# Kernel optimization log

Hardware: AMD Instinct MI355X
Metric: run time of the kernel (lower is better)

## Reference

```python
import jax, jax.numpy as jnp
import numpy as np

B, N, D = 2, 2048, 768
H = 12
HD = D // H
HID = 4 * D
SCALE = HD ** -0.5
EPS = 1e-5


def layer_norm(x, g, b):
    mu = jnp.mean(x, axis=-1, keepdims=True)
    var = jnp.var(x, axis=-1, keepdims=True)
    return (x - mu) * jax.lax.rsqrt(var + EPS) * g + b


def setup_inputs() -> dict:
    key = jax.random.key(0)
    ks = jax.random.split(key, 12)
    s = 0.02
    return {
        "x": jax.random.normal(ks[0], (B, N, D), jnp.float32),
        "att_mask": jax.random.randint(ks[1], (B, N), 0, 2, jnp.int32),
        "ln1_g": jnp.ones((D,), jnp.float32),
        "ln1_b": jnp.zeros((D,), jnp.float32),
        "qkv_w": jax.random.normal(ks[2], (3 * D, D), jnp.float32) * s,
        "q_bias": jnp.zeros((D,), jnp.float32),
        "v_bias": jnp.zeros((D,), jnp.float32),
        "proj_w": jax.random.normal(ks[3], (D, D), jnp.float32) * s,
        "proj_b": jnp.zeros((D,), jnp.float32),
        "ln2_g": jnp.ones((D,), jnp.float32),
        "ln2_b": jnp.zeros((D,), jnp.float32),
        "fc1_w": jax.random.normal(ks[4], (HID, D), jnp.float32) * s,
        "fc1_b": jnp.zeros((HID,), jnp.float32),
        "fc2_w": jax.random.normal(ks[5], (D, HID), jnp.float32) * s,
        "fc2_b": jnp.zeros((D,), jnp.float32),
        "gamma_1": 0.1 * jnp.ones((D,), jnp.float32),
        "gamma_2": 0.1 * jnp.ones((D,), jnp.float32),
    }


def reference(x, att_mask, ln1_g, ln1_b, qkv_w, q_bias, v_bias, proj_w, proj_b,
              ln2_g, ln2_b, fc1_w, fc1_b, fc2_w, fc2_b, gamma_1, gamma_2):
    # --- attention branch ---
    h = layer_norm(x, ln1_g, ln1_b)
    qkv_bias = jnp.concatenate([q_bias, jnp.zeros_like(v_bias), v_bias])
    qkv = h @ qkv_w.T + qkv_bias                      # [B,N,3D]
    qkv = qkv.reshape(B, N, 3, H, HD).transpose(2, 0, 3, 1, 4)
    q, k, v = qkv[0], qkv[1], qkv[2]                  # [B,H,N,HD]
    logit = jnp.einsum('bhqd,bhkd->bhqk', q * SCALE, k)
    mask = att_mask[:, None, None, :]                 # key mask [B,1,1,N]
    logit = jnp.where(mask == 0, -jnp.inf, logit)
    attn = jax.nn.softmax(logit, axis=-1)
    o = jnp.einsum('bhqk,bhkd->bhqd', attn, v)
    o = o.transpose(0, 2, 1, 3).reshape(B, N, D)
    o = o @ proj_w.T + proj_b
    x = x + gamma_1 * o
    # --- mlp branch ---
    h2 = layer_norm(x, ln2_g, ln2_b)
    h2 = jax.nn.gelu(h2 @ fc1_w.T + fc1_b, approximate=False)
    h2 = h2 @ fc2_w.T + fc2_b
    return x + gamma_2 * h2
```

## Files before the change

kernel.cpp:

```cpp
#include <hip/hip_runtime.h>
#include <hip/hip_bf16.h>
#include <stdint.h>

typedef __bf16 bf16x8 __attribute__((ext_vector_type(8)));
typedef __bf16 bf16x2 __attribute__((ext_vector_type(2)));
typedef unsigned short u16x8 __attribute__((ext_vector_type(8)));
typedef float f32x4 __attribute__((ext_vector_type(4)));
typedef float f32x16 __attribute__((ext_vector_type(16)));
typedef uint32_t u32x4 __attribute__((ext_vector_type(4)));

#define DMODEL 768
#define NSEQ   2048
#define BATCH  2
#define NHEAD  12
#define HDIM   64
#define HIDDEN 3072
#define PROWS  (BATCH * NHEAD * NSEQ)
#define NZ     4
#define QSCALE 0.18033688011112042f
#define MCONST 16.0f
#define PMASKED 1.52587890625e-05f

__device__ __forceinline__ uint16_t f2bf(float f) {
  __bf16 h = (__bf16)f;
  return __builtin_bit_cast(uint16_t, h);
}
__device__ __forceinline__ float bf2f(uint16_t u) {
  uint32_t x = (uint32_t)u << 16;
  return __builtin_bit_cast(float, x);
}
__device__ __forceinline__ bf16x8 ldb8(const uint16_t* p) {
  return __builtin_bit_cast(bf16x8, *reinterpret_cast<const u16x8*>(p));
}
__device__ __forceinline__ float gelu_f(float x) {
  float u = x * (1.0f + 0.044715f * x * x);
  float e = fminf(u * 2.302208545f, 80.0f);
  float t = exp2f(e);
  return x * t / (t + 1.0f);
}
__device__ __forceinline__ void xcd_swz(int& bx, int& by) {
  const int gx = gridDim.x;
  const int nwg = gx * gridDim.y;
  const int orig = blockIdx.y * gx + blockIdx.x;
  const int wg = (orig & 7) * (nwg >> 3) + (orig >> 3);
  bx = wg % gx;
  by = wg / gx;
}

using as1_void = __attribute__((address_space(1))) const void;
using as3_void = __attribute__((address_space(3))) void;
__device__ __forceinline__ void gload16(const uint16_t* src, uint16_t* lds) {
  __builtin_amdgcn_global_load_lds((as1_void*)src, (as3_void*)lds, 16, 0, 0);
}
#define MEMFENCE asm volatile("" ::: "memory")

#define N_QKVW  (3 * DMODEL * DMODEL)
#define N_PROJW (DMODEL * DMODEL)
#define N_FC1W  (HIDDEN * DMODEL)
#define N_FC2W  (DMODEL * HIDDEN)
__global__ __launch_bounds__(256) void cvt4_kernel(const float* __restrict__ s0,
                                                   const float* __restrict__ s1,
                                                   const float* __restrict__ s2,
                                                   const float* __restrict__ s3,
                                                   uint16_t* __restrict__ d0,
                                                   uint16_t* __restrict__ d1,
                                                   uint16_t* __restrict__ d2,
                                                   uint16_t* __restrict__ d3) {
  int i4 = (blockIdx.x * 256 + threadIdx.x) * 4;
  const float* s;
  uint16_t* d;
  if (i4 < N_QKVW) { s = s0 + i4; d = d0 + i4; }
  else if (i4 < N_QKVW + N_PROJW) { int j = i4 - N_QKVW; s = s1 + j; d = d1 + j; }
  else if (i4 < N_QKVW + N_PROJW + N_FC1W) { int j = i4 - N_QKVW - N_PROJW; s = s2 + j; d = d2 + j; }
  else { int j = i4 - N_QKVW - N_PROJW - N_FC1W; s = s3 + j; d = d3 + j; }
  float4 v = *reinterpret_cast<const float4*>(s);
  ushort4 o;
  o.x = f2bf(v.x); o.y = f2bf(v.y); o.z = f2bf(v.z); o.w = f2bf(v.w);
  *reinterpret_cast<ushort4*>(d) = o;
}

__global__ __launch_bounds__(256) void bias_kernel(const float* __restrict__ qb,
                                                   const float* __restrict__ vb,
                                                   float* __restrict__ out) {
  int j = blockIdx.x * 256 + threadIdx.x;
  if (j < 3 * DMODEL) {
    float v = 0.f;
    if (j < DMODEL) v = qb[j];
    else if (j >= 2 * DMODEL) v = vb[j - 2 * DMODEL];
    out[j] = v;
  }
}

__global__ __launch_bounds__(256) void ln_kernel(const float* __restrict__ x,
                                                 const float* __restrict__ g,
                                                 const float* __restrict__ bt,
                                                 uint16_t* __restrict__ out) {
  const int row = blockIdx.x;
  const int t = threadIdx.x;
  const float* xr = x + (size_t)row * DMODEL;
  float v0 = xr[t], v1 = xr[t + 256], v2 = xr[t + 512];
  float s = v0 + v1 + v2;
  float q = v0 * v0 + v1 * v1 + v2 * v2;
  for (int off = 32; off >= 1; off >>= 1) {
    s += __shfl_xor(s, off);
    q += __shfl_xor(q, off);
  }
  __shared__ float ss[4], sq[4];
  int w = t >> 6;
  if ((t & 63) == 0) { ss[w] = s; sq[w] = q; }
  __syncthreads();
  s = ss[0] + ss[1] + ss[2] + ss[3];
  q = sq[0] + sq[1] + sq[2] + sq[3];
  const float mean = s * (1.0f / DMODEL);
  const float var = q * (1.0f / DMODEL) - mean * mean;
  const float rstd = rsqrtf(var + 1e-5f);
  uint16_t* orow = out + (size_t)row * DMODEL;
  orow[t]       = f2bf((v0 - mean) * rstd * g[t]       + bt[t]);
  orow[t + 256] = f2bf((v1 - mean) * rstd * g[t + 256] + bt[t + 256]);
  orow[t + 512] = f2bf((v2 - mean) * rstd * g[t + 512] + bt[t + 512]);
}

template <int MODE>
__global__ __launch_bounds__(256, 3) void gemm128(const uint16_t* __restrict__ A,
                                                  const uint16_t* __restrict__ W,
                                                  const float* __restrict__ bias,
                                                  void* __restrict__ outp,
                                                  uint16_t* __restrict__ km,
                                                  uint16_t* __restrict__ vt,
                                                  const int* __restrict__ amask,
                                                  int M, int N, int K) {
  __shared__ uint16_t As[2][128 * 32];
  __shared__ uint16_t Bs[2][128 * 32];
  const int tid = threadIdx.x;
  const int lane = tid & 63;
  const int w = tid >> 6;
  const int wr = w >> 1, wc = w & 1;
  int bx, by;
  xcd_swz(bx, by);
  const int row0 = by * 128;
  const int col0 = bx * 128;
  const int lr = lane & 15;
  const int g = lane >> 4;

  const int o0 = w * 1024 + lane * 16;
  const int o1 = o0 + 4096;
  const int r0s = o0 >> 6, c0s = (o0 & 63) >> 1;
  const int r1s = o1 >> 6, c1s = (o1 & 63) >> 1;
  const int l0 = (w * 1024) >> 1;
  const int l1 = l0 + 2048;
  const uint16_t* Abase = A + (size_t)row0 * K;
  const uint16_t* Wbase = W + (size_t)col0 * K;

  auto stage = [&](int kt) {
    uint16_t* Ad = &As[kt & 1][0];
    uint16_t* Bd = &Bs[kt & 1][0];
    const int kk = kt * 32;
    gload16(Abase + (size_t)r0s * K + kk + c0s, Ad + l0);
    gload16(Abase + (size_t)r1s * K + kk + c1s, Ad + l1);
    gload16(Wbase + (size_t)r0s * K + kk + c0s, Bd + l0);
    gload16(Wbase + (size_t)r1s * K + kk + c1s, Bd + l1);
  };

  f32x4 acc[4][4] = {};
  const int nt = K >> 5;
  stage(0);
  for (int kt = 0; kt < nt; ++kt) {
    if (kt + 1 < nt) {
      stage(kt + 1);
      asm volatile("s_waitcnt vmcnt(4)" ::: "memory");
    } else {
      asm volatile("s_waitcnt vmcnt(0)" ::: "memory");
    }
    __builtin_amdgcn_s_barrier();
    MEMFENCE;
    const uint16_t* Ab = &As[kt & 1][0];
    const uint16_t* Bb = &Bs[kt & 1][0];
    bf16x8 a[4], b[4];
#pragma unroll
    for (int m = 0; m < 4; ++m) a[m] = ldb8(Ab + (wr * 64 + m * 16 + lr) * 32 + g * 8);
#pragma unroll
    for (int n = 0; n < 4; ++n) b[n] = ldb8(Bb + (wc * 64 + n * 16 + lr) * 32 + g * 8);
#pragma unroll
    for (int m = 0; m < 4; ++m)
#pragma unroll
      for (int n = 0; n < 4; ++n)
        acc[m][n] = __builtin_amdgcn_mfma_f32_16x16x32_bf16(a[m], b[n], acc[m][n], 0, 0, 0);
    MEMFENCE;
    __builtin_amdgcn_s_barrier();
  }

  if constexpr (MODE == 0) {
    const int sect = col0 / DMODEL;
    const int bb = row0 >> 11;
    const int* mrow = amask + bb * NSEQ;
#pragma unroll
    for (int m = 0; m < 4; ++m) {
      int row = row0 + wr * 64 + m * 16 + g * 4;
      int nn = row & 2047;
      int mk[4];
#pragma unroll
      for (int ri = 0; ri < 4; ++ri) mk[ri] = mrow[nn + ri];
#pragma unroll
      for (int n = 0; n < 4; ++n) {
        int col = col0 + wc * 64 + n * 16 + lr;
        float bv = bias[col];
        if (sect == 0) {
#pragma unroll
          for (int ri = 0; ri < 4; ++ri)
            ((uint16_t*)outp)[(size_t)(row + ri) * DMODEL + col] =
                f2bf((acc[m][n][ri] + bv) * QSCALE);
        } else if (sect == 1) {
          int kc = col - DMODEL;
#pragma unroll
          for (int ri = 0; ri < 4; ++ri)
            km[(size_t)(row + ri) * DMODEL + kc] =
                mk[ri] ? f2bf(acc[m][n][ri] + bv) : (uint16_t)0;
        } else {
          int vc = col - 2 * DMODEL;
          int hh2 = vc >> 6, dd = vc & 63;
          ushort4 sv;
          sv.x = mk[0] ? f2bf(acc[m][n][0] + bv) : (uint16_t)0;
          sv.y = mk[1] ? f2bf(acc[m][n][1] + bv) : (uint16_t)0;
          sv.z = mk[2] ? f2bf(acc[m][n][2] + bv) : (uint16_t)0;
          sv.w = mk[3] ? f2bf(acc[m][n][3] + bv) : (uint16_t)0;
          *reinterpret_cast<ushort4*>(
              vt + ((size_t)((bb * NHEAD + hh2) * 64 + dd)) * NSEQ + nn) = sv;
        }
      }
    }
  } else {
#pragma unroll
    for (int m = 0; m < 4; ++m) {
      int row = row0 + wr * 64 + m * 16 + g * 4;
#pragma unroll
      for (int n = 0; n < 4; ++n) {
        int col = col0 + wc * 64 + n * 16 + lr;
        float bv = bias[col];
#pragma unroll
        for (int ri = 0; ri < 4; ++ri) {
          float val = acc[m][n][ri] + bv;
          ((uint16_t*)outp)[(size_t)(row + ri) * N + col] = f2bf(gelu_f(val));
        }
      }
    }
  }
}

__global__ __launch_bounds__(256, 3) void gemm64(const uint16_t* __restrict__ A,
                                                 const uint16_t* __restrict__ W,
                                                 const float* __restrict__ bias,
                                                 float* __restrict__ outp,
                                                 const float* __restrict__ resid,
                                                 const float* __restrict__ gamma,
                                                 int M, int N, int K) {
  __shared__ uint16_t As[2][64 * 64];
  __shared__ uint16_t Bs[2][64 * 64];
  const int tid = threadIdx.x;
  const int lane = tid & 63;
  const int w = tid >> 6;
  const int wr = w >> 1, wc = w & 1;
  int bx, by;
  xcd_swz(bx, by);
  const int row0 = by * 64;
  const int col0 = bx * 64;
  const int lr = lane & 15;
  const int g = lane >> 4;

  const int srow = tid >> 3;
  const int schunk = tid & 7;
  const uint16_t* Abase = A + (size_t)row0 * K;
  const uint16_t* Wbase = W + (size_t)col0 * K;

  auto stage = [&](int kt) {
    uint16_t* Ad = &As[kt & 1][0];
    uint16_t* Bd = &Bs[kt & 1][0];
    const int kk = kt * 64;
#pragma unroll
    for (int i = 0; i < 2; ++i) {
      const int row = i * 32 + srow;
      const int sc = (schunk ^ (row & 7)) * 8;
      gload16(Abase + (size_t)row * K + kk + sc, Ad + i * 2048 + w * 512);
      gload16(Wbase + (size_t)row * K + kk + sc, Bd + i * 2048 + w * 512);
    }
  };

  f32x4 acc[2][2] = {};
  const int nt = K >> 6;
  stage(0);
  for (int kt = 0; kt < nt; ++kt) {
    if (kt + 1 < nt) {
      stage(kt + 1);
      asm volatile("s_waitcnt vmcnt(4)" ::: "memory");
    } else {
      asm volatile("s_waitcnt vmcnt(0)" ::: "memory");
    }
    __builtin_amdgcn_s_barrier();
    MEMFENCE;
    const uint16_t* Ab = &As[kt & 1][0];
    const uint16_t* Bb = &Bs[kt & 1][0];
#pragma unroll
    for (int kk = 0; kk < 2; ++kk) {
      bf16x8 a[2], bf[2];
#pragma unroll
      for (int m = 0; m < 2; ++m) {
        const int row = wr * 32 + m * 16 + lr;
        a[m] = ldb8(Ab + row * 64 + (((kk * 4 + g) ^ (row & 7)) * 8));
      }
#pragma unroll
      for (int n = 0; n < 2; ++n) {
        const int row = wc * 32 + n * 16 + lr;
        bf[n] = ldb8(Bb + row * 64 + (((kk * 4 + g) ^ (row & 7)) * 8));
      }
#pragma unroll
      for (int m = 0; m < 2; ++m)
#pragma unroll
        for (int n = 0; n < 2; ++n)
          acc[m][n] = __builtin_amdgcn_mfma_f32_16x16x32_bf16(a[m], bf[n], acc[m][n], 0, 0, 0);
    }
    MEMFENCE;
    __builtin_amdgcn_s_barrier();
  }

#pragma unroll
  for (int m = 0; m < 2; ++m) {
    int row = row0 + wr * 32 + m * 16 + g * 4;
#pragma unroll
    for (int n = 0; n < 2; ++n) {
      int col = col0 + wc * 32 + n * 16 + lr;
      float bv = bias[col];
      float gv = gamma[col];
#pragma unroll
      for (int ri = 0; ri < 4; ++ri) {
        float val = acc[m][n][ri] + bv;
        size_t idx = (size_t)(row + ri) * N + col;
        outp[idx] = resid[idx] + gv * val;
      }
    }
  }
}

__global__ __launch_bounds__(512, 4) void attn_kernel(const uint16_t* __restrict__ qb_,
                                                      const uint16_t* __restrict__ km,
                                                      const uint16_t* __restrict__ vt,
                                                      const int* __restrict__ mask,
                                                      uint16_t* __restrict__ po,
                                                      float* __restrict__ pml) {
  __shared__ uint16_t Kb[4][64 * 64];
  __shared__ uint16_t Vb[4][64 * 64];
  __shared__ unsigned long long mbits[8];
  const int tid = threadIdx.x;
  const int lane = tid & 63;
  const int w = tid >> 6;
  const int bh = blockIdx.x;
  const int b = bh / NHEAD, hd = bh % NHEAD;
  const int z = blockIdx.z;
  const int kbase = z * 512;
  const int q0 = blockIdx.y * 256 + w * 32;
  const int l31 = lane & 31;
  const int hh = lane >> 5;

  const int* mb = mask + b * NSEQ;
  {
    unsigned long long bm = __ballot(mb[kbase + w * 64 + lane] != 0);
    if (lane == 0) mbits[w] = bm;
  }

  bf16x8 qa[4];
  const uint16_t* qptr = qb_ + (size_t)(b * NSEQ + q0 + l31) * DMODEL + hd * HDIM + hh * 8;
#pragma unroll
  for (int dblk = 0; dblk < 4; ++dblk) qa[dblk] = ldb8(qptr + dblk * 16);

  const uint16_t* kmb = km + (size_t)b * NSEQ * DMODEL + hd * HDIM;
  const uint16_t* vtb = vt + (size_t)bh * HDIM * NSEQ;

  __syncthreads();

  const int srow = tid >> 3;
  const int sxor = ((tid & 7) ^ (srow & 7)) * 8;
  auto stage = [&](int t) {
    const int pb = t & 3;
    const int k0 = kbase + t * 64;
    gload16(kmb + (size_t)(k0 + srow) * DMODEL + sxor, &Kb[pb][w * 512]);
    gload16(vtb + (size_t)srow * NSEQ + k0 + sxor, &Vb[pb][w * 512]);
  };

  u16x8 ones_u;
#pragma unroll
  for (int e = 0; e < 8; ++e) ones_u[e] = 0x3F80;
  const bf16x8 ones = __builtin_bit_cast(bf16x8, ones_u);

  f32x16 oacc[2] = {};
  f32x16 lacc = {};

  stage(0);
  stage(1);
  stage(2);
#pragma unroll
  for (int t = 0; t < 8; ++t) {
    if (t < 6) {
      asm volatile("s_waitcnt vmcnt(4)" ::: "memory");
    } else if (t == 6) {
      asm volatile("s_waitcnt vmcnt(2)" ::: "memory");
    } else {
      asm volatile("s_waitcnt vmcnt(0)" ::: "memory");
    }
    __builtin_amdgcn_s_barrier();
    MEMFENCE;
    if (t + 3 < 8) stage(t + 3);
    const uint16_t* Kbp = &Kb[t & 3][0];
    const uint16_t* Vbp = &Vb[t & 3][0];

    f32x16 st[2];
    __builtin_amdgcn_s_setprio(1);
#pragma unroll
    for (int kblk = 0; kblk < 2; ++kblk) {
      f32x16 acc = {};
      const uint16_t* kr = Kbp + (kblk * 32 + l31) * 64;
#pragma unroll
      for (int dblk = 0; dblk < 4; ++dblk) {
        bf16x8 kf = ldb8(kr + ((dblk * 2 + hh) ^ (l31 & 7)) * 8);
        acc = __builtin_amdgcn_mfma_f32_32x32x16_bf16(kf, qa[dblk], acc, 0, 0, 0);
      }
      st[kblk] = acc;
    }
    __builtin_amdgcn_s_setprio(0);

    uint32_t pk[2][8];
#pragma unroll
    for (int kblk = 0; kblk < 2; ++kblk)
#pragma unroll
      for (int wn = 0; wn < 8; ++wn) {
        float e0 = exp2f(st[kblk][2 * wn] - MCONST);
        float e1 = exp2f(st[kblk][2 * wn + 1] - MCONST);
        bf16x2 pr = {(__bf16)e0, (__bf16)e1};
        pk[kblk][wn] = __builtin_bit_cast(uint32_t, pr);
      }

    bf16x8 af[4];
#pragma unroll
    for (int kb16 = 0; kb16 < 4; ++kb16) {
      const int kblk = kb16 >> 1;
      const int a4 = (kb16 & 1) * 4;
      uint32_t ow0 = hh ? pk[kblk][a4 + 2] : pk[kblk][a4 + 0];
      uint32_t ow1 = hh ? pk[kblk][a4 + 3] : pk[kblk][a4 + 1];
      uint32_t gv0 = hh ? pk[kblk][a4 + 0] : pk[kblk][a4 + 2];
      uint32_t gv1 = hh ? pk[kblk][a4 + 1] : pk[kblk][a4 + 3];
      uint32_t sw0 = (uint32_t)__shfl_xor((int)gv0, 32);
      uint32_t sw1 = (uint32_t)__shfl_xor((int)gv1, 32);
      u32x4 afu;
      afu[0] = hh ? sw0 : ow0;
      afu[1] = hh ? sw1 : ow1;
      afu[2] = hh ? ow0 : sw0;
      afu[3] = hh ? ow1 : sw1;
      af[kb16] = __builtin_bit_cast(bf16x8, afu);
    }

    __builtin_amdgcn_s_setprio(1);
#pragma unroll
    for (int dblk = 0; dblk < 2; ++dblk) {
      const uint16_t* vr = Vbp + (dblk * 32 + l31) * 64;
#pragma unroll
      for (int kb16 = 0; kb16 < 4; ++kb16) {
        bf16x8 vf = ldb8(vr + ((kb16 * 2 + hh) ^ (l31 & 7)) * 8);
        oacc[dblk] = __builtin_amdgcn_mfma_f32_32x32x16_bf16(af[kb16], vf, oacc[dblk], 0, 0, 0);
      }
    }
#pragma unroll
    for (int kb16 = 0; kb16 < 4; ++kb16)
      lacc = __builtin_amdgcn_mfma_f32_32x32x16_bf16(af[kb16], ones, lacc, 0, 0, 0);
    __builtin_amdgcn_s_setprio(0);
    MEMFENCE;
  }

  int cnt = 0;
#pragma unroll
  for (int it = 0; it < 8; ++it) cnt += 64 - __popcll(mbits[it]);
  const float cntf = (float)cnt * PMASKED;

  uint16_t* ob = po + ((size_t)z * PROWS + (size_t)bh * NSEQ + q0) * 64;
#pragma unroll
  for (int r = 0; r < 16; ++r) {
    const int qrow = (r & 3) + 8 * (r >> 2) + 4 * hh;
#pragma unroll
    for (int dblk = 0; dblk < 2; ++dblk)
      ob[(size_t)qrow * 64 + dblk * 32 + l31] = f2bf(oacc[dblk][r]);
  }
  if (l31 == 0) {
#pragma unroll
    for (int r = 0; r < 16; ++r) {
      const int qrow = (r & 3) + 8 * (r >> 2) + 4 * hh;
      pml[(size_t)z * PROWS + (size_t)bh * NSEQ + q0 + qrow] = lacc[r] - cntf;
    }
  }
}

__global__ __launch_bounds__(256) void merge_kernel(const uint16_t* __restrict__ po,
                                                    const float* __restrict__ pml,
                                                    uint16_t* __restrict__ o) {
  int gid = blockIdx.x * 256 + threadIdx.x;
  int row = gid >> 3;
  int c0 = (gid & 7) * 8;
  float L = 0.f;
#pragma unroll
  for (int zz = 0; zz < NZ; ++zz) L += pml[(size_t)zz * PROWS + row];
  float inv = L > 0.f ? 1.f / L : 0.f;
  float sum[8] = {};
#pragma unroll
  for (int zz = 0; zz < NZ; ++zz) {
    u16x8 a = *reinterpret_cast<const u16x8*>(po + ((size_t)zz * PROWS + row) * 64 + c0);
#pragma unroll
    for (int e = 0; e < 8; ++e) sum[e] += bf2f(a[e]);
  }
  int bh = row >> 11, q = row & 2047;
  int bb = bh / NHEAD, hh = bh % NHEAD;
  uint16_t* op = o + ((size_t)(bb * NSEQ + q) * DMODEL + hh * HDIM + c0);
  u16x8 outv;
#pragma unroll
  for (int e = 0; e < 8; ++e) outv[e] = f2bf(sum[e] * inv);
  *reinterpret_cast<u16x8*>(op) = outv;
}

extern "C" void kernel_launch(void* const* d_in, const int* in_sizes, int n_in,
                              void* d_out, int out_size, void* d_ws, size_t ws_size,
                              hipStream_t stream) {
  const float* x      = (const float*)d_in[0];
  const int*   amask  = (const int*)d_in[1];
  const float* ln1_g  = (const float*)d_in[2];
  const float* ln1_b  = (const float*)d_in[3];
  const float* qkv_w  = (const float*)d_in[4];
  const float* q_bias = (const float*)d_in[5];
  const float* v_bias = (const float*)d_in[6];
  const float* proj_w = (const float*)d_in[7];
  const float* proj_b = (const float*)d_in[8];
  const float* ln2_g  = (const float*)d_in[9];
  const float* ln2_b  = (const float*)d_in[10];
  const float* fc1_w  = (const float*)d_in[11];
  const float* fc1_b  = (const float*)d_in[12];
  const float* fc2_w  = (const float*)d_in[13];
  const float* fc2_b  = (const float*)d_in[14];
  const float* g1     = (const float*)d_in[15];
  const float* g2     = (const float*)d_in[16];

  char* ws = (char*)d_ws;
  uint16_t* qkvw_bf  = (uint16_t*)(ws + 0);
  uint16_t* projw_bf = (uint16_t*)(ws + 3538944);
  uint16_t* fc1w_bf  = (uint16_t*)(ws + 4718592);
  uint16_t* fc2w_bf  = (uint16_t*)(ws + 9437184);
  float*    qkvbias  = (float*)(ws + 14155776);
  uint16_t* h_bf     = (uint16_t*)(ws + 14164992);
  uint16_t* q_bf     = (uint16_t*)(ws + 20456448);
  uint16_t* km       = (uint16_t*)(ws + 26747904);
  uint16_t* vt_bf    = (uint16_t*)(ws + 33039360);
  uint16_t* po       = (uint16_t*)(ws + 39330816);
  float*    pml      = (float*)(ws + 64496640);
  uint16_t* o_bf     = q_bf;
  float*    x1_f     = (float*)(ws + 26747904);
  uint16_t* fc1_bf   = (uint16_t*)(ws + 39330816);
  uint16_t* h2_bf    = h_bf;

  const int M = BATCH * NSEQ;

  cvt4_kernel<<<(N_QKVW + N_PROJW + N_FC1W + N_FC2W) / 1024, 256, 0, stream>>>(
      qkv_w, proj_w, fc1_w, fc2_w, qkvw_bf, projw_bf, fc1w_bf, fc2w_bf);
  bias_kernel<<<(3 * DMODEL + 255) / 256, 256, 0, stream>>>(q_bias, v_bias, qkvbias);

  ln_kernel<<<M, 256, 0, stream>>>(x, ln1_g, ln1_b, h_bf);
  gemm128<0><<<dim3((3 * DMODEL) / 128, M / 128), 256, 0, stream>>>(
      h_bf, qkvw_bf, qkvbias, q_bf, km, vt_bf, amask, M, 3 * DMODEL, DMODEL);
  attn_kernel<<<dim3(BATCH * NHEAD, NSEQ / 256, NZ), 512, 0, stream>>>(
      q_bf, km, vt_bf, amask, po, pml);
  merge_kernel<<<(PROWS * 8) / 256, 256, 0, stream>>>(po, pml, o_bf);
  gemm64<<<dim3(DMODEL / 64, M / 64), 256, 0, stream>>>(
      o_bf, projw_bf, proj_b, x1_f, x, g1, M, DMODEL, DMODEL);
  ln_kernel<<<M, 256, 0, stream>>>(x1_f, ln2_g, ln2_b, h2_bf);
  gemm128<2><<<dim3(HIDDEN / 128, M / 128), 256, 0, stream>>>(
      h2_bf, fc1w_bf, fc1_b, fc1_bf, nullptr, nullptr, nullptr, M, HIDDEN, DMODEL);
  gemm64<<<dim3(DMODEL / 64, M / 64), 256, 0, stream>>>(
      fc1_bf, fc2w_bf, fc2_b, (float*)d_out, x1_f, g2, M, DMODEL, HIDDEN);
}
```

Baseline: 180.6 us.

## Compact unmasked keys so attention only iterates over valid key tiles

A new scan kernel computes prefix positions of unmasked keys per batch. The QKV GEMM epilogue scatters K and V rows into compacted positions, and the K/V buffers are zeroed beforehand. Attention then splits only the valid key tiles across its NZ partitions and corrects for padding in the denominator. With a random mask about half the keys are masked, so this is meant to roughly halve attention work, at the cost of extra memsets, a scan launch, and scattered scalar stores in the GEMM epilogue.

```diff
diff --git a/kernel.cpp b/kernel.cpp
--- a/kernel.cpp
+++ b/kernel.cpp
@@ -91,6 +91,31 @@
   }
 }
 
+__global__ __launch_bounds__(256) void scan_kernel(const int* __restrict__ mask,
+                                                   int* __restrict__ pos,
+                                                   int* __restrict__ nk) {
+  const int b = blockIdx.x;
+  const int tid = threadIdx.x;
+  const int lane = tid & 63, w = tid >> 6;
+  __shared__ int wsum[4];
+  int base = 0;
+  for (int c = 0; c < NSEQ; c += 256) {
+    int m = (mask[b * NSEQ + c + tid] != 0);
+    unsigned long long bits = __ballot(m);
+    int lanepre = __popcll(bits & ((1ull << lane) - 1ull));
+    if (lane == 0) wsum[w] = __popcll(bits);
+    __syncthreads();
+    int wpre = 0;
+#pragma unroll
+    for (int i = 0; i < 4; ++i) wpre += (i < w) ? wsum[i] : 0;
+    pos[b * NSEQ + c + tid] = base + wpre + lanepre;
+    int total = wsum[0] + wsum[1] + wsum[2] + wsum[3];
+    __syncthreads();
+    base += total;
+  }
+  if (tid == 0) nk[b] = base;
+}
+
 __global__ __launch_bounds__(256) void ln_kernel(const float* __restrict__ x,
                                                  const float* __restrict__ g,
                                                  const float* __restrict__ bt,
@@ -128,6 +153,7 @@
                                                   uint16_t* __restrict__ km,
                                                   uint16_t* __restrict__ vt,
                                                   const int* __restrict__ amask,
+                                                  const int* __restrict__ pos,
                                                   int M, int N, int K) {
   __shared__ uint16_t As[2][128 * 32];
   __shared__ uint16_t Bs[2][128 * 32];
@@ -193,13 +219,14 @@
     const int sect = col0 / DMODEL;
     const int bb = row0 >> 11;
     const int* mrow = amask + bb * NSEQ;
+    const int* prow = pos + bb * NSEQ;
 #pragma unroll
     for (int m = 0; m < 4; ++m) {
       int row = row0 + wr * 64 + m * 16 + g * 4;
       int nn = row & 2047;
-      int mk[4];
-#pragma unroll
-      for (int ri = 0; ri < 4; ++ri) mk[ri] = mrow[nn + ri];
+      int mk[4], ps[4];
+#pragma unroll
+      for (int ri = 0; ri < 4; ++ri) { mk[ri] = mrow[nn + ri]; ps[ri] = prow[nn + ri]; }
 #pragma unroll
       for (int n = 0; n < 4; ++n) {
         int col = col0 + wc * 64 + n * 16 + lr;
@@ -213,18 +240,15 @@
           int kc = col - DMODEL;
 #pragma unroll
           for (int ri = 0; ri < 4; ++ri)
-            km[(size_t)(row + ri) * DMODEL + kc] =
-                mk[ri] ? f2bf(acc[m][n][ri] + bv) : (uint16_t)0;
+            if (mk[ri])
+              km[(size_t)(bb * NSEQ + ps[ri]) * DMODEL + kc] = f2bf(acc[m][n][ri] + bv);
         } else {
           int vc = col - 2 * DMODEL;
           int hh2 = vc >> 6, dd = vc & 63;
-          ushort4 sv;
-          sv.x = mk[0] ? f2bf(acc[m][n][0] + bv) : (uint16_t)0;
-          sv.y = mk[1] ? f2bf(acc[m][n][1] + bv) : (uint16_t)0;
-          sv.z = mk[2] ? f2bf(acc[m][n][2] + bv) : (uint16_t)0;
-          sv.w = mk[3] ? f2bf(acc[m][n][3] + bv) : (uint16_t)0;
-          *reinterpret_cast<ushort4*>(
-              vt + ((size_t)((bb * NHEAD + hh2) * 64 + dd)) * NSEQ + nn) = sv;
+          const size_t vbase = (size_t)((bb * NHEAD + hh2) * 64 + dd) * NSEQ;
+#pragma unroll
+          for (int ri = 0; ri < 4; ++ri)
+            if (mk[ri]) vt[vbase + ps[ri]] = f2bf(acc[m][n][ri] + bv);
         }
       }
     }
@@ -342,28 +366,27 @@
 __global__ __launch_bounds__(512, 4) void attn_kernel(const uint16_t* __restrict__ qb_,
                                                       const uint16_t* __restrict__ km,
                                                       const uint16_t* __restrict__ vt,
-                                                      const int* __restrict__ mask,
+                                                      const int* __restrict__ nkarr,
                                                       uint16_t* __restrict__ po,
                                                       float* __restrict__ pml) {
   __shared__ uint16_t Kb[4][64 * 64];
   __shared__ uint16_t Vb[4][64 * 64];
-  __shared__ unsigned long long mbits[8];
   const int tid = threadIdx.x;
   const int lane = tid & 63;
   const int w = tid >> 6;
   const int bh = blockIdx.x;
   const int b = bh / NHEAD, hd = bh % NHEAD;
   const int z = blockIdx.z;
-  const int kbase = z * 512;
   const int q0 = blockIdx.y * 256 + w * 32;
   const int l31 = lane & 31;
   const int hh = lane >> 5;
 
-  const int* mb = mask + b * NSEQ;
-  {
-    unsigned long long bm = __ballot(mb[kbase + w * 64 + lane] != 0);
-    if (lane == 0) mbits[w] = bm;
-  }
+  const int NKb = nkarr[b];
+  const int NTt = (NKb + 63) >> 6;
+  const int TPZ = (NTt + NZ - 1) >> 2;
+  const int s0 = (z * TPZ < NTt) ? z * TPZ : NTt;
+  int e0 = s0 + TPZ; if (e0 > NTt) e0 = NTt;
+  const int nt = e0 - s0;
 
   bf16x8 qa[4];
   const uint16_t* qptr = qb_ + (size_t)(b * NSEQ + q0 + l31) * DMODEL + hd * HDIM + hh * 8;
@@ -372,14 +395,12 @@
 
   const uint16_t* kmb = km + (size_t)b * NSEQ * DMODEL + hd * HDIM;
   const uint16_t* vtb = vt + (size_t)bh * HDIM * NSEQ;
-
-  __syncthreads();
 
   const int srow = tid >> 3;
   const int sxor = ((tid & 7) ^ (srow & 7)) * 8;
   auto stage = [&](int t) {
     const int pb = t & 3;
-    const int k0 = kbase + t * 64;
+    const int k0 = t * 64;
     gload16(kmb + (size_t)(k0 + srow) * DMODEL + sxor, &Kb[pb][w * 512]);
     gload16(vtb + (size_t)srow * NSEQ + k0 + sxor, &Vb[pb][w * 512]);
   };
@@ -392,23 +413,23 @@
   f32x16 oacc[2] = {};
   f32x16 lacc = {};
 
-  stage(0);
-  stage(1);
-  stage(2);
-#pragma unroll
-  for (int t = 0; t < 8; ++t) {
-    if (t < 6) {
+  if (nt > 0) stage(s0);
+  if (nt > 1) stage(s0 + 1);
+  if (nt > 2) stage(s0 + 2);
+  for (int i = 0; i < nt; ++i) {
+    const int ahead = nt - 1 - i;
+    if (ahead >= 2) {
       asm volatile("s_waitcnt vmcnt(4)" ::: "memory");
-    } else if (t == 6) {
+    } else if (ahead == 1) {
       asm volatile("s_waitcnt vmcnt(2)" ::: "memory");
     } else {
       asm volatile("s_waitcnt vmcnt(0)" ::: "memory");
     }
     __builtin_amdgcn_s_barrier();
     MEMFENCE;
-    if (t + 3 < 8) stage(t + 3);
-    const uint16_t* Kbp = &Kb[t & 3][0];
-    const uint16_t* Vbp = &Vb[t & 3][0];
+    if (i + 3 < nt) stage(s0 + i + 3);
+    const uint16_t* Kbp = &Kb[(s0 + i) & 3][0];
+    const uint16_t* Vbp = &Vb[(s0 + i) & 3][0];
 
     f32x16 st[2];
     __builtin_amdgcn_s_setprio(1);
@@ -430,9 +451,9 @@
     for (int kblk = 0; kblk < 2; ++kblk)
 #pragma unroll
       for (int wn = 0; wn < 8; ++wn) {
-        float e0 = exp2f(st[kblk][2 * wn] - MCONST);
-        float e1 = exp2f(st[kblk][2 * wn + 1] - MCONST);
-        bf16x2 pr = {(__bf16)e0, (__bf16)e1};
+        float e0x = exp2f(st[kblk][2 * wn] - MCONST);
+        float e1x = exp2f(st[kblk][2 * wn + 1] - MCONST);
+        bf16x2 pr = {(__bf16)e0x, (__bf16)e1x};
         pk[kblk][wn] = __builtin_bit_cast(uint32_t, pr);
       }
 
@@ -472,10 +493,10 @@
     MEMFENCE;
   }
 
-  int cnt = 0;
-#pragma unroll
-  for (int it = 0; it < 8; ++it) cnt += 64 - __popcll(mbits[it]);
-  const float cntf = (float)cnt * PMASKED;
+  int vend = e0 * 64; if (vend > NKb) vend = NKb;
+  int valid = vend - s0 * 64; if (valid < 0) valid = 0;
+  const int pads = nt * 64 - valid;
+  const float cntf = (float)pads * PMASKED;
 
   uint16_t* ob = po + ((size_t)z * PROWS + (size_t)bh * NSEQ + q0) * 64;
 #pragma unroll
@@ -553,6 +574,8 @@
   uint16_t* vt_bf    = (uint16_t*)(ws + 33039360);
   uint16_t* po       = (uint16_t*)(ws + 39330816);
   float*    pml      = (float*)(ws + 64496640);
+  int*      posbuf   = (int*)(ws + 65283072);
+  int*      nkbuf    = (int*)(ws + 65299456);
   uint16_t* o_bf     = q_bf;
   float*    x1_f     = (float*)(ws + 26747904);
   uint16_t* fc1_bf   = (uint16_t*)(ws + 39330816);
@@ -563,18 +586,21 @@
   cvt4_kernel<<<(N_QKVW + N_PROJW + N_FC1W + N_FC2W) / 1024, 256, 0, stream>>>(
       qkv_w, proj_w, fc1_w, fc2_w, qkvw_bf, projw_bf, fc1w_bf, fc2w_bf);
   bias_kernel<<<(3 * DMODEL + 255) / 256, 256, 0, stream>>>(q_bias, v_bias, qkvbias);
+  scan_kernel<<<BATCH, 256, 0, stream>>>(amask, posbuf, nkbuf);
+  hipMemsetAsync(km, 0, (size_t)BATCH * NSEQ * DMODEL * 2, stream);
+  hipMemsetAsync(vt_bf, 0, (size_t)BATCH * NHEAD * HDIM * NSEQ * 2, stream);
 
   ln_kernel<<<M, 256, 0, stream>>>(x, ln1_g, ln1_b, h_bf);
   gemm128<0><<<dim3((3 * DMODEL) / 128, M / 128), 256, 0, stream>>>(
-      h_bf, qkvw_bf, qkvbias, q_bf, km, vt_bf, amask, M, 3 * DMODEL, DMODEL);
+      h_bf, qkvw_bf, qkvbias, q_bf, km, vt_bf, amask, posbuf, M, 3 * DMODEL, DMODEL);
   attn_kernel<<<dim3(BATCH * NHEAD, NSEQ / 256, NZ), 512, 0, stream>>>(
-      q_bf, km, vt_bf, amask, po, pml);
+      q_bf, km, vt_bf, nkbuf, po, pml);
   merge_kernel<<<(PROWS * 8) / 256, 256, 0, stream>>>(po, pml, o_bf);
   gemm64<<<dim3(DMODEL / 64, M / 64), 256, 0, stream>>>(
       o_bf, projw_bf, proj_b, x1_f, x, g1, M, DMODEL, DMODEL);
   ln_kernel<<<M, 256, 0, stream>>>(x1_f, ln2_g, ln2_b, h2_bf);
   gemm128<2><<<dim3(HIDDEN / 128, M / 128), 256, 0, stream>>>(
-      h2_bf, fc1w_bf, fc1_b, fc1_bf, nullptr, nullptr, nullptr, M, HIDDEN, DMODEL);
+      h2_bf, fc1w_bf, fc1_b, fc1_bf, nullptr, nullptr, nullptr, nullptr, M, HIDDEN, DMODEL);
   gemm64<<<dim3(DMODEL / 64, M / 64), 256, 0, stream>>>(
       fc1_bf, fc2w_bf, fc2_b, (float*)d_out, x1_f, g2, M, DMODEL, HIDDEN);
 }
```

Result: no change. 183.6 us (+1.7%).
